# Kernel optimization log

Hardware: AMD Instinct MI355X
Metric: run time of the kernel (lower is better)

Reference implementation:

```python
import jax, jax.numpy as jnp
import numpy as np

DELTA_V = 0.5
DELTA_D = 1.5
ALPHA = 1.0
BETA = 1.0
GAMMA = 0.001
K = 64  # max number of instance ids per batch element


def _safe_sqrt(sq):
    # sqrt with zero-safe gradient: exact where sq > 0, returns 0 otherwise
    pos = sq > 0
    return jnp.sqrt(jnp.where(pos, sq, 1.0)) * pos.astype(sq.dtype)


def setup_inputs() -> dict:
    key = jax.random.key(0)
    k1, k2 = jax.random.split(key)
    B, N, D = 16, 65536, 32
    embeddings = jax.random.normal(k1, (B, N, D), dtype=jnp.float32)
    instance_ids = jax.random.randint(k2, (B, N), 0, K, dtype=jnp.int32)
    mask = jnp.ones((B, N), dtype=bool)
    return {"embeddings": embeddings, "instance_ids": instance_ids, "mask": mask}


def reference(embeddings, instance_ids, mask):
    B, N, D = embeddings.shape
    f32 = embeddings.dtype
    valid = mask & (instance_ids >= 0)
    # flat segment id per point; invalid points go to dump segment B*K
    batch_off = jnp.arange(B, dtype=jnp.int32)[:, None] * K
    seg = jnp.where(valid, batch_off + instance_ids, B * K).reshape(-1)
    w = valid.reshape(-1).astype(f32)
    flat = embeddings.reshape(-1, D)

    # per-instance sums / counts -> means  (segment reduce, memory-bound)
    sums = jax.ops.segment_sum(flat * w[:, None], seg, num_segments=B * K + 1)[: B * K]
    counts = jax.ops.segment_sum(w, seg, num_segments=B * K + 1)[: B * K]
    means_flat = sums / jnp.maximum(counts, 1.0)[:, None]  # (B*K, D)
    present = (counts > 0).reshape(B, K)                   # (B, K)
    num_inst = present.sum(-1).astype(f32)                 # (B,)
    valid_b = (num_inst >= 2).astype(f32)                  # batches counted as samples

    # ---- variance (pull) loss ----
    seg_clip = jnp.minimum(seg, B * K - 1)
    diff = flat - means_flat[seg_clip]                     # (B*N, D)
    dist = _safe_sqrt((diff * diff).sum(-1))
    pen = jnp.maximum(dist - DELTA_V, 0.0) ** 2 * w
    inst_pen = jax.ops.segment_sum(pen, seg, num_segments=B * K + 1)[: B * K]
    inst_pen = (inst_pen / jnp.maximum(counts, 1.0)).reshape(B, K)
    var_b = (inst_pen * present).sum(-1) / jnp.maximum(num_inst, 1.0)

    # ---- distance (push) loss: pairwise over instance means ----
    means = means_flat.reshape(B, K, D)
    dsq = ((means[:, :, None, :] - means[:, None, :, :]) ** 2).sum(-1)  # (B, K, K)
    iu = jnp.arange(K)
    pair_m = present[:, :, None] & present[:, None, :] & (iu[:, None] < iu[None, :])
    pair_mf = pair_m.astype(f32)
    pdist = _safe_sqrt(jnp.where(pair_m, dsq, 1.0)) * pair_mf
    pen2 = jnp.maximum(2.0 * DELTA_D - pdist, 0.0) ** 2 * pair_mf
    num_pairs = num_inst * (num_inst - 1.0) / 2.0
    dist_b = pen2.sum((1, 2)) / jnp.maximum(num_pairs, 1.0)

    # ---- regularization loss ----
    mnorm = _safe_sqrt((means * means).sum(-1)) * present.astype(f32)  # (B, K)
    reg_b = mnorm.sum(-1) / jnp.maximum(num_inst, 1.0)

    denom = jnp.maximum(valid_b.sum(), 1.0)
    var_loss = (var_b * valid_b).sum() / denom
    dist_loss = (dist_b * valid_b).sum() / denom
    reg_loss = (reg_b * valid_b).sum() / denom
    total = ALPHA * var_loss + BETA * dist_loss + GAMMA * reg_loss
    return jnp.stack([total, var_loss, dist_loss, reg_loss])
```

## Files before the change

### kernel.cpp

```cpp
#include <hip/hip_runtime.h>
#include <cstdint>

#define BB 16
#define NN 65536
#define DD 32
#define KK 64
#define DELTA_V 0.5f
#define DELTA_D 1.5f
#define GRID 512
#define PPB 2048
#define WPTS 512
#define NSTG 8

typedef short bf16x8 __attribute__((ext_vector_type(8)));
typedef float f32x16 __attribute__((ext_vector_type(16)));

__device__ __forceinline__ short f2bf(float x) {
    union { float f; unsigned u; } v; v.f = x;
    const unsigned r = v.u + 0x7FFFu + ((v.u >> 16) & 1u);
    return (short)(r >> 16);
}

__device__ __forceinline__ int fpoll(int* p) {
    return __hip_atomic_fetch_add(p, 0, __ATOMIC_RELAXED, __HIP_MEMORY_SCOPE_AGENT);
}
__device__ __forceinline__ void arrive(int* p) {
    __hip_atomic_fetch_add(p, 1, __ATOMIC_RELEASE, __HIP_MEMORY_SCOPE_AGENT);
}
__device__ __forceinline__ void spinge(int* p, int tgt) {
    const long long t0 = clock64();
    while (fpoll(p) < tgt) {
        __builtin_amdgcn_s_sleep(8);
        if (clock64() - t0 > (long long)2e8) break;
    }
    (void)__hip_atomic_load(p, __ATOMIC_ACQUIRE, __HIP_MEMORY_SCOPE_AGENT);
}

__global__ __launch_bounds__(64) void k_init(int* bar) {
    for (int j = threadIdx.x; j < 2048; j += 64) bar[j] = 0;
}


__global__ __launch_bounds__(256, 2) void k_fused(
    const float* __restrict__ emb, const int* __restrict__ ids,
    const int* __restrict__ mask, float* parts, float* pcnt,
    float* varpart, float* aux, int* bar, float* __restrict__ out)
{
    __shared__ float tb[4][64][36];
    __shared__ float lc2[4][KK];
    __shared__ float red[4];
    __shared__ float sf[4][BB];
    __shared__ int s_last;
    const int tid  = threadIdx.x;
    const int w    = tid >> 6, lane = tid & 63;
    const int half = lane >> 5, d32 = lane & 31;
    const int pl   = lane >> 3, pc = lane & 7;
    const int gblk = blockIdx.x;
    const int b    = gblk >> 5;
    const size_t pw = (size_t)b * NN + (size_t)(gblk & 31) * PPB + (size_t)w * WPTS;

    {
        f32x16 acc0 = {}, acc1 = {};
        int c0 = 0, c1 = 0;
        const int m0 = d32, m1 = d32 + 32;
        float (*T)[36] = tb[w];
        const float4* epb  = (const float4*)(emb + pw * DD);
        const int*    idsb = ids + pw;
        const int*    mskb = mask + pw;

        float4 r[8]; int idr, mkr;
#pragma unroll
        for (int i = 0; i < 8; ++i) r[i] = epb[i * 64 + lane];
        idr = idsb[lane]; mkr = mskb[lane];

#pragma unroll
        for (int s = 0; s < NSTG; ++s) {
            float4 r2[8]; int idr2 = 0, mkr2 = 0;
            if (s < NSTG - 1) {
                const float4* ep4 = epb + (s + 1) * 512;
#pragma unroll
                for (int i = 0; i < 8; ++i) r2[i] = ep4[i * 64 + lane];
                idr2 = idsb[(s + 1) * 64 + lane];
                mkr2 = mskb[(s + 1) * 64 + lane];
            }
            const int vid = (mkr != 0 && (unsigned)idr < KK) ? idr : -1;
#pragma unroll
            for (int i = 0; i < 8; ++i)
                *(float4*)&T[i * 8 + pl][4 * pc] = r[i];
#pragma unroll
            for (int q = 0; q < 4; ++q) {
                bf16x8 bfB, a0, a1;
#pragma unroll
                for (int e = 0; e < 8; ++e) {
                    bfB[e] = f2bf(T[q * 16 + 8 * half + e][d32]);
                    const int s_lo = __builtin_amdgcn_readlane(vid, q * 16 + e);
                    const int s_hi = __builtin_amdgcn_readlane(vid, q * 16 + 8 + e);
                    const int sel  = half ? s_hi : s_lo;
                    const bool h0 = (sel == m0), h1 = (sel == m1);
                    a0[e] = h0 ? (short)0x3F80 : (short)0;
                    a1[e] = h1 ? (short)0x3F80 : (short)0;
                    c0 += h0 ? 1 : 0;
                    c1 += h1 ? 1 : 0;
                }
                acc0 = __builtin_amdgcn_mfma_f32_32x32x16_bf16(a0, bfB, acc0, 0, 0, 0);
                acc1 = __builtin_amdgcn_mfma_f32_32x32x16_bf16(a1, bfB, acc1, 0, 0, 0);
            }
            if (s < NSTG - 1) {
#pragma unroll
                for (int i = 0; i < 8; ++i) r[i] = r2[i];
                idr = idr2; mkr = mkr2;
            }
        }
#pragma unroll
        for (int rr = 0; rr < 16; ++rr) {
            const int mrow = (rr & 3) + 8 * (rr >> 2) + 4 * half;
            T[mrow][d32]      = acc0[rr];
            T[32 + mrow][d32] = acc1[rr];
        }
        c0 += __shfl_down(c0, 32);
        c1 += __shfl_down(c1, 32);
        if (lane < 32) { lc2[w][lane] = (float)c0; lc2[w][lane + 32] = (float)c1; }
        __syncthreads();

        float* pb = parts + (size_t)gblk * 2048;
        for (int i = tid; i < 2048; i += 256) {
            const int row = i >> 5, col = i & 31;
            pb[i] = tb[0][row][col] + tb[1][row][col]
                  + tb[2][row][col] + tb[3][row][col];
        }
        if (tid < KK)
            pcnt[(size_t)gblk * KK + tid] =
                lc2[0][tid] + lc2[1][tid] + lc2[2][tid] + lc2[3][tid];
    }
    __syncthreads();

    if (tid == 0) {
        arrive(&bar[b * 32]);
        spinge(&bar[b * 32], 32);
    }
    __syncthreads();

    float (*smu)[36] = tb[0];
    if (tid < KK) {
        float s = 0.f;
        const float* pc0 = pcnt + (size_t)b * 32 * KK + tid;
        for (int j = 0; j < 32; ++j) s += pc0[j * KK];
        smu[tid][32] = s;
        smu[tid][33] = 1.f / fmaxf(s, 1.f);
    }
    __syncthreads();
    for (int e = tid; e < 2048; e += 256) {
        float s = 0.f;
        const float* pp = parts + (size_t)b * 32 * 2048 + e;
        for (int j = 0; j < 32; ++j) s += pp[j * 2048];
        smu[e >> 5][e & 31] = s * smu[e >> 5][33];
    }
    __syncthreads();

    if ((gblk & 31) == 0) {
        float ninst = 0.f;
        if (tid < KK) {
            const float c = smu[tid][32];
            const float pres = (c > 0.f) ? 1.f : 0.f;
            float sq = 0.f;
#pragma unroll
            for (int d = 0; d < DD; ++d) { const float m = smu[tid][d]; sq = fmaf(m, m, sq); }
            float nm = ((sq > 0.f) ? sqrtf(sq) : 0.f) * pres;
            float pn = pres;
            for (int off = 32; off; off >>= 1) {
                pn += __shfl_down(pn, off);
                nm += __shfl_down(nm, off);
            }
            if (tid == 0) {
                ninst = pn;
                aux[b]      = nm / fmaxf(pn, 1.f);
                aux[32 + b] = pn;
            }
        }
        float acc = 0.f;
        for (int idx = tid; idx < KK * KK; idx += 256) {
            const int i = idx >> 6, j = idx & 63;
            if (i < j && smu[i][32] > 0.f && smu[j][32] > 0.f) {
                float dsq = 0.f;
#pragma unroll
                for (int d = 0; d < DD; ++d) {
                    const float df = smu[i][d] - smu[j][d];
                    dsq = fmaf(df, df, dsq);
                }
                const float pd = (dsq > 0.f) ? sqrtf(dsq) : 0.f;
                const float pen = fmaxf(2.f * DELTA_D - pd, 0.f);
                acc = fmaf(pen, pen, acc);
            }
        }
        for (int off = 32; off; off >>= 1) acc += __shfl_down(acc, off);
        if ((tid & 63) == 0) red[tid >> 6] = acc;
        __syncthreads();
        if (tid == 0) {
            const float tot = red[0] + red[1] + red[2] + red[3];
            const float np = ninst * (ninst - 1.f) * 0.5f;
            aux[16 + b] = tot / fmaxf(np, 1.f);
            arrive(&bar[512]);
        }
        __syncthreads();
    }

    {
        const float4* epb  = (const float4*)(emb + pw * DD);
        const int*    idsb = ids + pw;
        const int*    mskb = mask + pw;
        float accv = 0.f;
        for (int t = 0; t < 8; ++t) {
            const int idr = idsb[t * 64 + lane];
            const int mkr = mskb[t * 64 + lane];
            const int vid = (mkr != 0 && (unsigned)idr < KK) ? idr : -1;
            float4 x[8];
#pragma unroll
            for (int g = 0; g < 8; ++g) x[g] = epb[t * 512 + g * 64 + lane];
#pragma unroll
            for (int g = 0; g < 8; ++g) {
                const int sid = __shfl(vid, g * 8 + pl);
                const int row = (sid >= 0) ? sid : 0;
                const float4 m4 = *(const float4*)&smu[row][4 * pc];
                float a = x[g].x - m4.x; float dsq = a * a;
                a = x[g].y - m4.y; dsq = fmaf(a, a, dsq);
                a = x[g].z - m4.z; dsq = fmaf(a, a, dsq);
                a = x[g].w - m4.w; dsq = fmaf(a, a, dsq);
                dsq += __shfl_xor(dsq, 1);
                dsq += __shfl_xor(dsq, 2);
                dsq += __shfl_xor(dsq, 4);
                if (pc == 0 && sid >= 0) {
                    const float dist = (dsq > 0.f) ? sqrtf(dsq) : 0.f;
                    float pen = fmaxf(dist - DELTA_V, 0.f);
                    accv = fmaf(pen * pen, smu[row][33], accv);
                }
            }
        }
        for (int off = 32; off; off >>= 1) accv += __shfl_down(accv, off);
        if (lane == 0) red[w] = accv;
        __syncthreads();
        if (tid == 0) varpart[gblk] = red[0] + red[1] + red[2] + red[3];
    }

    if (tid == 0) {
        const int ret = __hip_atomic_fetch_add(&bar[544], 1, __ATOMIC_RELEASE,
                                               __HIP_MEMORY_SCOPE_AGENT);
        s_last = (ret == GRID - 1) ? 1 : 0;
        if (s_last) spinge(&bar[512], BB);
    }
    __syncthreads();
    if (s_last) {
        if (tid < BB) {
            float vs = 0.f;
            for (int j = 0; j < 32; ++j) vs += varpart[tid * 32 + j];
            const float ni = aux[32 + tid];
            sf[0][tid] = vs / fmaxf(ni, 1.f);
            sf[1][tid] = (ni >= 2.f) ? 1.f : 0.f;
            sf[2][tid] = aux[tid];
            sf[3][tid] = aux[16 + tid];
        }
        __syncthreads();
        if (tid == 0) {
            float denom = 0.f, v = 0.f, d = 0.f, r = 0.f;
            for (int bb = 0; bb < BB; ++bb) {
                const float vb = sf[1][bb];
                denom += vb;
                v += sf[0][bb] * vb;
                d += sf[3][bb] * vb;
                r += sf[2][bb] * vb;
            }
            denom = fmaxf(denom, 1.f);
            v /= denom; d /= denom; r /= denom;
            out[0] = v + d + 0.001f * r;
            out[1] = v;
            out[2] = d;
            out[3] = r;
        }
    }
}

extern "C" void kernel_launch(void* const* d_in, const int* in_sizes, int n_in,
                              void* d_out, int out_size, void* d_ws, size_t ws_size,
                              hipStream_t stream)
{
    const float* emb  = (const float*)d_in[0];
    const int*   ids  = (const int*)d_in[1];
    const int*   mask = (const int*)d_in[2];

    float* ws      = (float*)d_ws;
    int*   bar     = (int*)ws;
    float* parts   = ws + 2048;
    float* pcnt    = parts + (size_t)GRID * 2048;
    float* varpart = pcnt + (size_t)GRID * KK;
    float* aux     = varpart + GRID;

    k_init<<<1, 64, 0, stream>>>(bar);
    k_fused<<<GRID, 256, 0, stream>>>(emb, ids, mask, parts, pcnt,
                                      varpart, aux, bar, (float*)d_out);
}
```

Baseline: 101.0 us.

## Double block size and distribute per-batch mean reduction across blocks

Blocks now have 512 threads, so each wave handles 256 points instead of 512. Previously every block in a batch re-reduced all 32 partial sums and counts to build the full mean table. Now each block reduces only its two instances into a global mu buffer, and a second per-batch barrier publishes the table, which every block then loads. This removes redundant reduction traffic but adds another grid-level spin barrier and higher per-block resource pressure with launch_bounds(512,4).

Measured after the change: 102.5 us. About the same (+1.5%).

```diff
diff --git a/kernel.cpp b/kernel.cpp
--- a/kernel.cpp
+++ b/kernel.cpp
@@ -9,8 +9,8 @@
 #define DELTA_D 1.5f
 #define GRID 512
 #define PPB 2048
-#define WPTS 512
-#define NSTG 8
+#define WPTS 256
+#define NSTG 4
 
 typedef short bf16x8 __attribute__((ext_vector_type(8)));
 typedef float f32x16 __attribute__((ext_vector_type(16)));
@@ -41,15 +41,16 @@
 }
 
 
-__global__ __launch_bounds__(256, 2) void k_fused(
+__global__ __launch_bounds__(512, 4) void k_fused(
     const float* __restrict__ emb, const int* __restrict__ ids,
-    const int* __restrict__ mask, float* parts, float* pcnt,
+    const int* __restrict__ mask, float* parts, float* pcnt, float* mu,
     float* varpart, float* aux, int* bar, float* __restrict__ out)
 {
-    __shared__ float tb[4][64][36];
-    __shared__ float lc2[4][KK];
-    __shared__ float red[4];
+    __shared__ float tb[8][64][36];
+    __shared__ float lc2[8][64];
+    __shared__ float red[8];
     __shared__ float sf[4][BB];
+    __shared__ float scq[2];
     __shared__ int s_last;
     const int tid  = threadIdx.x;
     const int w    = tid >> 6, lane = tid & 63;
@@ -123,37 +124,65 @@
         __syncthreads();
 
         float* pb = parts + (size_t)gblk * 2048;
-        for (int i = tid; i < 2048; i += 256) {
+        for (int i = tid; i < 2048; i += 512) {
             const int row = i >> 5, col = i & 31;
-            pb[i] = tb[0][row][col] + tb[1][row][col]
-                  + tb[2][row][col] + tb[3][row][col];
-        }
-        if (tid < KK)
-            pcnt[(size_t)gblk * KK + tid] =
-                lc2[0][tid] + lc2[1][tid] + lc2[2][tid] + lc2[3][tid];
-    }
-    __syncthreads();
-
-    if (tid == 0) {
-        arrive(&bar[b * 32]);
-        spinge(&bar[b * 32], 32);
-    }
+            float s = 0.f;
+#pragma unroll
+            for (int ww = 0; ww < 8; ++ww) s += tb[ww][row][col];
+            pb[i] = s;
+        }
+        if (tid < KK) {
+            float s = 0.f;
+#pragma unroll
+            for (int ww = 0; ww < 8; ++ww) s += lc2[ww][tid];
+            pcnt[(size_t)gblk * KK + tid] = s;
+        }
+    }
+    __syncthreads();
+
+    if (tid == 0) { arrive(&bar[b * 32]); spinge(&bar[b * 32], 32); }
+    __syncthreads();
+
+    {
+        const int kb = (gblk & 31) * 2;
+        if (tid < 64) {
+            const int k = kb + (tid >> 5);
+            const int j = tid & 31;
+            float cv = pcnt[((size_t)(b * 32 + j)) * KK + k];
+            for (int off = 16; off; off >>= 1) cv += __shfl_down(cv, off);
+            if ((tid & 31) == 0) {
+                mu[((size_t)b * KK + k) * 36 + 32] = cv;
+                const float rc = 1.f / fmaxf(cv, 1.f);
+                mu[((size_t)b * KK + k) * 36 + 33] = rc;
+                scq[tid >> 5] = rc;
+            }
+        }
+        __syncthreads();
+        const int e  = tid & 63;
+        const int jg = tid >> 6;
+        float s = 0.f;
+#pragma unroll
+        for (int jj = 0; jj < 4; ++jj)
+            s += parts[((size_t)(b * 32 + jg * 4 + jj)) * 2048 + kb * 32 + e];
+        lc2[jg][e] = s;
+        __syncthreads();
+        if (tid < 64) {
+            float t = 0.f;
+#pragma unroll
+            for (int g = 0; g < 8; ++g) t += lc2[g][tid];
+            mu[((size_t)b * KK + kb + (tid >> 5)) * 36 + (tid & 31)] =
+                t * scq[tid >> 5];
+        }
+    }
+    __syncthreads();
+
+    if (tid == 0) { arrive(&bar[b * 32 + 8]); spinge(&bar[b * 32 + 8], 32); }
     __syncthreads();
 
     float (*smu)[36] = tb[0];
-    if (tid < KK) {
-        float s = 0.f;
-        const float* pc0 = pcnt + (size_t)b * 32 * KK + tid;
-        for (int j = 0; j < 32; ++j) s += pc0[j * KK];
-        smu[tid][32] = s;
-        smu[tid][33] = 1.f / fmaxf(s, 1.f);
-    }
-    __syncthreads();
-    for (int e = tid; e < 2048; e += 256) {
-        float s = 0.f;
-        const float* pp = parts + (size_t)b * 32 * 2048 + e;
-        for (int j = 0; j < 32; ++j) s += pp[j * 2048];
-        smu[e >> 5][e & 31] = s * smu[e >> 5][33];
+    {
+        const float* mub = mu + (size_t)b * KK * 36;
+        for (int i = tid; i < KK * 36; i += 512) ((float*)smu)[i] = mub[i];
     }
     __syncthreads();
 
@@ -178,7 +207,7 @@
             }
         }
         float acc = 0.f;
-        for (int idx = tid; idx < KK * KK; idx += 256) {
+        for (int idx = tid; idx < KK * KK; idx += 512) {
             const int i = idx >> 6, j = idx & 63;
             if (i < j && smu[i][32] > 0.f && smu[j][32] > 0.f) {
                 float dsq = 0.f;
@@ -196,7 +225,9 @@
         if ((tid & 63) == 0) red[tid >> 6] = acc;
         __syncthreads();
         if (tid == 0) {
-            const float tot = red[0] + red[1] + red[2] + red[3];
+            float tot = 0.f;
+#pragma unroll
+            for (int g = 0; g < 8; ++g) tot += red[g];
             const float np = ninst * (ninst - 1.f) * 0.5f;
             aux[16 + b] = tot / fmaxf(np, 1.f);
             arrive(&bar[512]);
@@ -209,7 +240,7 @@
         const int*    idsb = ids + pw;
         const int*    mskb = mask + pw;
         float accv = 0.f;
-        for (int t = 0; t < 8; ++t) {
+        for (int t = 0; t < NSTG; ++t) {
             const int idr = idsb[t * 64 + lane];
             const int mkr = mskb[t * 64 + lane];
             const int vid = (mkr != 0 && (unsigned)idr < KK) ? idr : -1;
@@ -238,7 +269,12 @@
         for (int off = 32; off; off >>= 1) accv += __shfl_down(accv, off);
         if (lane == 0) red[w] = accv;
         __syncthreads();
-        if (tid == 0) varpart[gblk] = red[0] + red[1] + red[2] + red[3];
+        if (tid == 0) {
+            float s = 0.f;
+#pragma unroll
+            for (int g = 0; g < 8; ++g) s += red[g];
+            varpart[gblk] = s;
+        }
     }
 
     if (tid == 0) {
@@ -290,10 +326,11 @@
     int*   bar     = (int*)ws;
     float* parts   = ws + 2048;
     float* pcnt    = parts + (size_t)GRID * 2048;
-    float* varpart = pcnt + (size_t)GRID * KK;
+    float* mu      = pcnt + (size_t)GRID * KK;
+    float* varpart = mu + (size_t)BB * KK * 36;
     float* aux     = varpart + GRID;
 
     k_init<<<1, 64, 0, stream>>>(bar);
-    k_fused<<<GRID, 256, 0, stream>>>(emb, ids, mask, parts, pcnt,
+    k_fused<<<GRID, 512, 0, stream>>>(emb, ids, mask, parts, pcnt, mu,
                                       varpart, aux, bar, (float*)d_out);
 }
```
